# Kernel optimization log

Hardware: AMD Instinct MI355X
Metric: run time of the kernel (lower is better)

The kernel has to match this reference:

```python
import jax, jax.numpy as jnp
import numpy as np

EPS = 1e-3  # tfa LayerNormLSTMCell default norm epsilon

def _ln(z, g, b):
    # layernorm over last axis, per gate: z [B,4,U], g/b [4,U]
    mu = jnp.mean(z, axis=-1, keepdims=True)
    var = jnp.mean((z - mu) ** 2, axis=-1, keepdims=True)
    return g * (z - mu) * jax.lax.rsqrt(var + EPS) + b

def setup_inputs() -> dict:
    key = jax.random.key(0)
    ks = jax.random.split(key, 12)
    B, T, D, U, C = 1024, 100, 300, 512, 14
    sc = lambda k, shape, fan: jax.random.normal(k, shape, jnp.float32) * (1.0 / np.sqrt(fan))
    return {
        "x": jax.random.normal(ks[0], (B, T, D), jnp.float32),
        "mask": jax.random.randint(ks[1], (B, T), 0, 2).astype(jnp.int32),
        # layer 0 (input dim D)
        "W0": sc(ks[2], (D, 4 * U), D), "U0": sc(ks[3], (U, 4 * U), U),
        "b0": jnp.zeros((4 * U,), jnp.float32),
        "g0": jnp.ones((4, U), jnp.float32), "be0": jnp.zeros((4, U), jnp.float32),
        # layer 1 (input dim U)
        "W1": sc(ks[4], (U, 4 * U), U), "U1": sc(ks[5], (U, 4 * U), U),
        "b1": jnp.zeros((4 * U,), jnp.float32),
        "g1": jnp.ones((4, U), jnp.float32), "be1": jnp.zeros((4, U), jnp.float32),
        # dense softmax head
        "Wd": sc(ks[6], (U, C), U), "bd": jnp.zeros((C,), jnp.float32),
    }

def reference(x, mask, W0, U0, b0, g0, be0, W1, U1, b1, g1, be1, Wd, bd):
    B, T, D = x.shape
    U = W0.shape[1] // 4
    params = [(W0, U0, b0, g0, be0), (W1, U1, b1, g1, be1)]

    def step(carry, tins):
        hs, cs = carry
        xt, mt = tins                      # xt [B,D_in], mt [B]
        m = (mt > 0)[:, None]
        inp = xt
        new_hs, new_cs = [], []
        for l in range(2):
            W, Uw, b, g, be = params[l]
            z = (inp @ W + hs[l] @ Uw).reshape(B, 4, U)
            z = _ln(z, g, be) + b.reshape(4, U)
            i_g = jax.nn.sigmoid(z[:, 0])
            f_g = jax.nn.sigmoid(z[:, 1])
            c_g = jnp.tanh(z[:, 2])
            o_g = jax.nn.sigmoid(z[:, 3])
            c = f_g * cs[l] + i_g * c_g
            h = o_g * jnp.tanh(c)
            # keras RNN masking: carry state through masked steps
            h = jnp.where(m, h, hs[l])
            c = jnp.where(m, c, cs[l])
            new_hs.append(h); new_cs.append(c)
            inp = h
        return (tuple(new_hs), tuple(new_cs)), None

    z0 = jnp.zeros((B, U), x.dtype)
    carry0 = ((z0, z0), (z0, z0))
    xs = (jnp.swapaxes(x, 0, 1), mask.T)   # time-major [T,B,...]
    (hs, _), _ = jax.lax.scan(step, carry0, xs)
    h_top = hs[-1]                          # [B,U] = last valid output via mask carry
    return jax.nn.softmax(h_top @ Wd + bd, axis=-1)
```

## Files before the change

### kernel.cpp

```cpp
#include <hip/hip_runtime.h>


typedef _Float16 f16;
typedef _Float16 f16x8 __attribute__((ext_vector_type(8)));
typedef float f32x4 __attribute__((ext_vector_type(4)));

__global__ __launch_bounds__(256) void convert_x(
    const float* __restrict__ x, long lda, f16* __restrict__ xh, int rows) {
  int idx = blockIdx.x * 256 + threadIdx.x;
  if (idx >= rows * 320) return;
  int row = idx / 320, k = idx - row * 320;
  xh[idx] = (k < 300) ? (f16)x[(long)row * lda + k] : (f16)0.f;
}

__global__ __launch_bounds__(256) void transpose_f16(
    const float* __restrict__ W, f16* __restrict__ Bt, int K, int N, int Kp) {
  __shared__ float s[32][33];
  int n0 = blockIdx.x * 32, k0 = blockIdx.y * 32;
  int tid = threadIdx.x, c = tid & 31, r8 = tid >> 5;
  for (int rr = r8; rr < 32; rr += 8) {
    int k = k0 + rr;
    s[rr][c] = (k < K) ? W[(long)k * N + (n0 + c)] : 0.0f;
  }
  __syncthreads();
  for (int rr = r8; rr < 32; rr += 8)
    Bt[(long)(n0 + rr) * Kp + (k0 + c)] = (f16)s[c][rr];
}

__global__ __launch_bounds__(256) void gemm_f16(
    const f16* __restrict__ A1, long lda1, int K1, const f16* __restrict__ B1,
    const f16* __restrict__ A2, long lda2, int K2, const f16* __restrict__ B2,
    float* __restrict__ Zf) {
  int tid = threadIdx.x;
  int lane = tid & 63, w = tid >> 6;
  int l15 = lane & 15, quad = lane >> 4;
  long bn0 = (long)blockIdx.x * 128 + w * 32;
  long bm0 = (long)blockIdx.y * 64;

  f32x4 acc[4][2] = {};

  for (int pass = 0; pass < 2; ++pass) {
    int K = pass ? K2 : K1;
    if (K == 0) continue;
    const f16* A = pass ? A2 : A1;
    const f16* Bt = pass ? B2 : B1;
    long lda = pass ? lda2 : lda1;
    const f16* a0 = A + (bm0 + l15) * lda + quad * 8;
    const f16* b0 = Bt + (bn0 + l15) * (long)K + quad * 8;

    for (int k0 = 0; k0 < K; k0 += 32) {
      f16x8 af[4], bf[2];
#pragma unroll
      for (int i = 0; i < 4; ++i)
        af[i] = *(const f16x8*)(a0 + (long)i * 16 * lda + k0);
#pragma unroll
      for (int j = 0; j < 2; ++j)
        bf[j] = *(const f16x8*)(b0 + (long)j * 16 * K + k0);
#pragma unroll
      for (int i = 0; i < 4; ++i)
#pragma unroll
        for (int j = 0; j < 2; ++j)
          acc[i][j] = __builtin_amdgcn_mfma_f32_16x16x32_f16(af[i], bf[j], acc[i][j], 0, 0, 0);
    }
  }

#pragma unroll
  for (int i = 0; i < 4; ++i) {
    long row = bm0 + i * 16 + quad * 4;
#pragma unroll
    for (int j = 0; j < 2; ++j) {
      long col = bn0 + j * 16 + l15;
#pragma unroll
      for (int r = 0; r < 4; ++r)
        Zf[(row + r) * 2048 + col] = acc[i][j][r];
    }
  }
}

#define LOADF(AF, BF, A0, B0, K0)                          \
  AF[0] = *(const f16x8*)((A0) + (K0));                    \
  AF[1] = *(const f16x8*)((A0) + 16 * 512 + (K0));         \
  AF[2] = *(const f16x8*)((A0) + 32 * 512 + (K0));         \
  AF[3] = *(const f16x8*)((A0) + 48 * 512 + (K0));         \
  BF[0] = *(const f16x8*)((B0) + (K0));                    \
  BF[1] = *(const f16x8*)((B0) + 16 * 512 + (K0));

#define MFMAS(AF, BF)                                                                   \
  acc[0][0] = __builtin_amdgcn_mfma_f32_16x16x32_f16(AF[0], BF[0], acc[0][0], 0, 0, 0); \
  acc[0][1] = __builtin_amdgcn_mfma_f32_16x16x32_f16(AF[0], BF[1], acc[0][1], 0, 0, 0); \
  acc[1][0] = __builtin_amdgcn_mfma_f32_16x16x32_f16(AF[1], BF[0], acc[1][0], 0, 0, 0); \
  acc[1][1] = __builtin_amdgcn_mfma_f32_16x16x32_f16(AF[1], BF[1], acc[1][1], 0, 0, 0); \
  acc[2][0] = __builtin_amdgcn_mfma_f32_16x16x32_f16(AF[2], BF[0], acc[2][0], 0, 0, 0); \
  acc[2][1] = __builtin_amdgcn_mfma_f32_16x16x32_f16(AF[2], BF[1], acc[2][1], 0, 0, 0); \
  acc[3][0] = __builtin_amdgcn_mfma_f32_16x16x32_f16(AF[3], BF[0], acc[3][0], 0, 0, 0); \
  acc[3][1] = __builtin_amdgcn_mfma_f32_16x16x32_f16(AF[3], BF[1], acc[3][1], 0, 0, 0);

__global__ __launch_bounds__(256, 2) void gemm_step(
    const float* __restrict__ xt,
    const f16* __restrict__ h0, const f16* __restrict__ h1,
    const f16* __restrict__ W0t,
    const f16* __restrict__ U0t, const f16* __restrict__ W1t,
    const f16* __restrict__ U1t,
    float* __restrict__ zA, float* __restrict__ zB, int do0, int do1) {
  int prob = blockIdx.y >> 4;
  if (prob ? !do1 : !do0) return;
  int tid = threadIdx.x;
  int lane = tid & 63, w = tid >> 6;
  int l15 = lane & 15, quad = lane >> 4;
  long bn0 = (long)blockIdx.x * 128 + w * 32;
  long bm0 = (long)(blockIdx.y & 15) * 64;
  long arow = (bm0 + l15) * 512 + quad * 8;
  long brow = (bn0 + l15) * 512 + quad * 8;

  f32x4 acc[4][2] = {};

  if (prob == 0) {
    {
      const float* ax = xt + (bm0 + l15) * 30000L + quad * 8;
      const f16* bw = W0t + (bn0 + l15) * 320L + quad * 8;
#pragma unroll
      for (int k0 = 0; k0 < 288; k0 += 32) {
        f16x8 af[4], bf[2];
#pragma unroll
        for (int i = 0; i < 4; ++i) {
          f32x4 lo = *(const f32x4*)(ax + (long)i * 480000 + k0);
          f32x4 hi = *(const f32x4*)(ax + (long)i * 480000 + k0 + 4);
#pragma unroll
          for (int e = 0; e < 4; ++e) {
            af[i][e] = (f16)lo[e];
            af[i][4 + e] = (f16)hi[e];
          }
        }
        bf[0] = *(const f16x8*)(bw + k0);
        bf[1] = *(const f16x8*)(bw + 16 * 320 + k0);
        MFMAS(af, bf)
      }
      {
        f16x8 af[4], bf[2];
#pragma unroll
        for (int i = 0; i < 4; ++i) {
          long rb = (bm0 + l15 + i * 16) * 30000L;
#pragma unroll
          for (int e = 0; e < 8; ++e) {
            int k = 288 + quad * 8 + e;
            af[i][e] = (k < 300) ? (f16)xt[rb + k] : (f16)0.f;
          }
        }
        bf[0] = *(const f16x8*)(bw + 288);
        bf[1] = *(const f16x8*)(bw + 16 * 320 + 288);
        MFMAS(af, bf)
      }
    }
    {
      const f16* a0 = h0 + arow;
      const f16* b0 = U0t + brow;
      f16x8 af0[4], bf0[2], af1[4], bf1[2];
      LOADF(af0, bf0, a0, b0, 0)
      for (int k0 = 0; k0 < 448; k0 += 64) {
        LOADF(af1, bf1, a0, b0, k0 + 32)
        MFMAS(af0, bf0)
        LOADF(af0, bf0, a0, b0, k0 + 64)
        MFMAS(af1, bf1)
      }
      LOADF(af1, bf1, a0, b0, 480)
      MFMAS(af0, bf0)
      MFMAS(af1, bf1)
    }
  } else {
    const f16* ax = h0 + arow;
    const f16* bx = W1t + brow;
    const f16* ay = h1 + arow;
    const f16* by = U1t + brow;
    f16x8 axf0[4], bxf0[2], axf1[4], bxf1[2];
    f16x8 ayf0[4], byf0[2], ayf1[4], byf1[2];
    LOADF(axf0, bxf0, ax, bx, 0)
    LOADF(ayf0, byf0, ay, by, 0)
    for (int k0 = 0; k0 < 448; k0 += 64) {
      LOADF(axf1, bxf1, ax, bx, k0 + 32)
      LOADF(ayf1, byf1, ay, by, k0 + 32)
      MFMAS(axf0, bxf0)
      MFMAS(ayf0, byf0)
      LOADF(axf0, bxf0, ax, bx, k0 + 64)
      LOADF(ayf0, byf0, ay, by, k0 + 64)
      MFMAS(axf1, bxf1)
      MFMAS(ayf1, byf1)
    }
    LOADF(axf1, bxf1, ax, bx, 480)
    LOADF(ayf1, byf1, ay, by, 480)
    MFMAS(axf0, bxf0)
    MFMAS(ayf0, byf0)
    MFMAS(axf1, bxf1)
    MFMAS(ayf1, byf1)
  }

  float* Z = prob ? zB : zA;
#pragma unroll
  for (int i = 0; i < 4; ++i) {
    long row = bm0 + i * 16 + quad * 4;
#pragma unroll
    for (int j = 0; j < 2; ++j) {
      long col = bn0 + j * 16 + l15;
#pragma unroll
      for (int r = 0; r < 4; ++r)
        Z[(row + r) * 2048 + col] = acc[i][j][r];
    }
  }
}

__global__ __launch_bounds__(256) void ln_gates(
    const float* __restrict__ z, const float* __restrict__ gamma,
    const float* __restrict__ beta, const float* __restrict__ bias,
    const int* __restrict__ mask, int t,
    f16* __restrict__ h, float* __restrict__ c) {
  __shared__ float act[2048];
  int b = blockIdx.x;
  int tid = threadIdx.x;
  int w = tid >> 6, lane = tid & 63;

  const float* zb = z + (long)b * 2048 + w * 512;
  float zv[8];
  float sum = 0.0f, sq = 0.0f;
#pragma unroll
  for (int i = 0; i < 8; ++i) {
    float v = zb[lane + 64 * i];
    zv[i] = v;
    sum += v;
    sq += v * v;
  }
#pragma unroll
  for (int off = 32; off; off >>= 1) {
    sum += __shfl_xor(sum, off);
    sq += __shfl_xor(sq, off);
  }
  float mu = sum * (1.0f / 512.0f);
  float var = sq * (1.0f / 512.0f) - mu * mu;
  float is = rsqrtf(var + 1e-3f);

#pragma unroll
  for (int i = 0; i < 8; ++i) {
    int k = lane + 64 * i;
    float val = gamma[w * 512 + k] * (zv[i] - mu) * is + beta[w * 512 + k] + bias[w * 512 + k];
    float a;
    if (w == 2) {
      a = 2.0f / (1.0f + __expf(-2.0f * val)) - 1.0f;
    } else {
      a = 1.0f / (1.0f + __expf(-val));
    }
    act[w * 512 + k] = a;
  }
  __syncthreads();

  bool m = mask[(long)b * 100 + t] > 0;
#pragma unroll
  for (int i = 0; i < 2; ++i) {
    int u = tid + 256 * i;
    float co = c[(long)b * 512 + u];
    float ho = (float)h[(long)b * 512 + u];
    float cn = act[512 + u] * co + act[u] * act[1024 + u];
    float th = 2.0f / (1.0f + __expf(-2.0f * cn)) - 1.0f;
    float hn = act[1536 + u] * th;
    h[(long)b * 512 + u] = (f16)(m ? hn : ho);
    c[(long)b * 512 + u] = m ? cn : co;
  }
}

__global__ __launch_bounds__(256) void ln_gates2(
    const float* __restrict__ zA, const float* __restrict__ zB,
    const float* __restrict__ g0, const float* __restrict__ be0,
    const float* __restrict__ b0, const float* __restrict__ g1,
    const float* __restrict__ be1, const float* __restrict__ b1,
    const int* __restrict__ mask, int t,
    f16* __restrict__ h0, float* __restrict__ c0,
    f16* __restrict__ h1, float* __restrict__ c1, int do0, int do1) {
  __shared__ float act[2048];
  int layer = blockIdx.x >> 10;
  if (layer ? !do1 : !do0) return;
  int b = blockIdx.x & 1023;
  const float* z = layer ? zB : zA;
  const float* gamma = layer ? g1 : g0;
  const float* beta = layer ? be1 : be0;
  const float* bias = layer ? b1 : b0;
  f16* h = layer ? h1 : h0;
  float* c = layer ? c1 : c0;
  int tm = layer ? (t - 1) : t;

  int tid = threadIdx.x;
  int w = tid >> 6, lane = tid & 63;

  const float* zb = z + (long)b * 2048 + w * 512;
  float zv[8];
  float sum = 0.0f, sq = 0.0f;
#pragma unroll
  for (int i = 0; i < 8; ++i) {
    float v = zb[lane + 64 * i];
    zv[i] = v;
    sum += v;
    sq += v * v;
  }
#pragma unroll
  for (int off = 32; off; off >>= 1) {
    sum += __shfl_xor(sum, off);
    sq += __shfl_xor(sq, off);
  }
  float mu = sum * (1.0f / 512.0f);
  float var = sq * (1.0f / 512.0f) - mu * mu;
  float is = rsqrtf(var + 1e-3f);

#pragma unroll
  for (int i = 0; i < 8; ++i) {
    int k = lane + 64 * i;
    float val = gamma[w * 512 + k] * (zv[i] - mu) * is + beta[w * 512 + k] + bias[w * 512 + k];
    float a;
    if (w == 2) {
      a = 2.0f / (1.0f + __expf(-2.0f * val)) - 1.0f;
    } else {
      a = 1.0f / (1.0f + __expf(-val));
    }
    act[w * 512 + k] = a;
  }
  __syncthreads();

  bool m = mask[(long)b * 100 + tm] > 0;
#pragma unroll
  for (int i = 0; i < 2; ++i) {
    int u = tid + 256 * i;
    float co = c[(long)b * 512 + u];
    float ho = (float)h[(long)b * 512 + u];
    float cn = act[512 + u] * co + act[u] * act[1024 + u];
    float th = 2.0f / (1.0f + __expf(-2.0f * cn)) - 1.0f;
    float hn = act[1536 + u] * th;
    h[(long)b * 512 + u] = (f16)(m ? hn : ho);
    c[(long)b * 512 + u] = m ? cn : co;
  }
}

__global__ __launch_bounds__(64) void head_kernel(
    const f16* __restrict__ h, const float* __restrict__ Wd,
    const float* __restrict__ bd, float* __restrict__ out) {
  __shared__ float hs[512];
  __shared__ float lg[16];
  int b = blockIdx.x, tid = threadIdx.x;
#pragma unroll
  for (int i = 0; i < 8; ++i) hs[tid + 64 * i] = (float)h[(long)b * 512 + tid + 64 * i];
  __syncthreads();
  if (tid < 14) {
    float s = bd[tid];
    for (int k = 0; k < 512; ++k) s += hs[k] * Wd[k * 14 + tid];
    lg[tid] = s;
  }
  __syncthreads();
  if (tid < 14) {
    float mx = lg[0];
#pragma unroll
    for (int i = 1; i < 14; ++i) mx = fmaxf(mx, lg[i]);
    float e = __expf(lg[tid] - mx);
    float den = 0.0f;
#pragma unroll
    for (int i = 0; i < 14; ++i) den += __expf(lg[i] - mx);
    out[(long)b * 14 + tid] = e / den;
  }
}

extern "C" void kernel_launch(void* const* d_in, const int* in_sizes, int n_in,
                              void* d_out, int out_size, void* d_ws, size_t ws_size,
                              hipStream_t stream) {
  const float* x   = (const float*)d_in[0];
  const int* mask  = (const int*)d_in[1];
  const float* W0  = (const float*)d_in[2];
  const float* U0w = (const float*)d_in[3];
  const float* b0  = (const float*)d_in[4];
  const float* g0  = (const float*)d_in[5];
  const float* be0 = (const float*)d_in[6];
  const float* W1  = (const float*)d_in[7];
  const float* U1w = (const float*)d_in[8];
  const float* b1  = (const float*)d_in[9];
  const float* g1  = (const float*)d_in[10];
  const float* be1 = (const float*)d_in[11];
  const float* Wd  = (const float*)d_in[12];
  const float* bd  = (const float*)d_in[13];
  float* out = (float*)d_out;

  char* p = (char*)d_ws;
  f16*   h0  = (f16*)(p + 0);
  f16*   h1  = (f16*)(p + ((size_t)1 << 20));
  float* c0  = (float*)(p + ((size_t)2 << 20));
  float* c1  = (float*)(p + ((size_t)4 << 20));
  float* zA  = (float*)(p + ((size_t)6 << 20));
  f16*   W0t = (f16*)(p + ((size_t)14 << 20));
  f16*   U0t = (f16*)(p + ((size_t)14 << 20) + 1310720);
  f16*   W1t = (f16*)(p + ((size_t)14 << 20) + 1310720 + 2097152);
  f16*   U1t = (f16*)(p + ((size_t)14 << 20) + 1310720 + 2 * 2097152);
  float* zB  = (float*)(p + ((size_t)22 << 20));
  f16*   xh  = (f16*)(p + ((size_t)22 << 20));

  const bool pipe = ws_size >= ((size_t)30 << 20);

  hipMemsetAsync(p, 0, (size_t)6 << 20, stream);

  transpose_f16<<<dim3(64, 10), 256, 0, stream>>>(W0,  W0t, 300, 2048, 320);
  transpose_f16<<<dim3(64, 16), 256, 0, stream>>>(U0w, U0t, 512, 2048, 512);
  transpose_f16<<<dim3(64, 16), 256, 0, stream>>>(W1,  W1t, 512, 2048, 512);
  transpose_f16<<<dim3(64, 16), 256, 0, stream>>>(U1w, U1t, 512, 2048, 512);

  if (pipe) {
    for (int t = 0; t <= 100; ++t) {
      int do0 = (t < 100) ? 1 : 0;
      int do1 = (t >= 1) ? 1 : 0;
      gemm_step<<<dim3(16, 32), 256, 0, stream>>>(
          x + (long)t * 300, h0, h1, W0t, U0t, W1t, U1t, zA, zB, do0, do1);
      ln_gates2<<<2048, 256, 0, stream>>>(
          zA, zB, g0, be0, b0, g1, be1, b1, mask, t, h0, c0, h1, c1, do0, do1);
    }
  } else {
    for (int t = 0; t < 100; ++t) {
      convert_x<<<(1024 * 320 + 255) / 256, 256, 0, stream>>>(x + (long)t * 300, 30000, xh, 1024);
      gemm_f16<<<dim3(16, 16), 256, 0, stream>>>(
          xh, 320, 320, W0t, h0, 512, 512, U0t, zA);
      ln_gates<<<1024, 256, 0, stream>>>(zA, g0, be0, b0, mask, t, h0, c0);
      gemm_f16<<<dim3(16, 16), 256, 0, stream>>>(
          h0, 512, 512, W1t, h1, 512, 512, U1t, zA);
      ln_gates<<<1024, 256, 0, stream>>>(zA, g1, be1, b1, mask, t, h1, c1);
    }
  }

  head_kernel<<<1024, 64, 0, stream>>>(h1, Wd, bd, out);
}
```

Before: 5.768 ms.

## Hoist layer-0 input projection out of recurrence and fuse layer-1 weights

```diff
diff --git a/kernel.cpp b/kernel.cpp
--- a/kernel.cpp
+++ b/kernel.cpp
@@ -5,16 +5,9 @@
 typedef _Float16 f16x8 __attribute__((ext_vector_type(8)));
 typedef float f32x4 __attribute__((ext_vector_type(4)));
 
-__global__ __launch_bounds__(256) void convert_x(
-    const float* __restrict__ x, long lda, f16* __restrict__ xh, int rows) {
-  int idx = blockIdx.x * 256 + threadIdx.x;
-  if (idx >= rows * 320) return;
-  int row = idx / 320, k = idx - row * 320;
-  xh[idx] = (k < 300) ? (f16)x[(long)row * lda + k] : (f16)0.f;
-}
-
 __global__ __launch_bounds__(256) void transpose_f16(
-    const float* __restrict__ W, f16* __restrict__ Bt, int K, int N, int Kp) {
+    const float* __restrict__ W, f16* __restrict__ Bt, int K, int N, int Kp,
+    int k_off) {
   __shared__ float s[32][33];
   int n0 = blockIdx.x * 32, k0 = blockIdx.y * 32;
   int tid = threadIdx.x, c = tid & 31, r8 = tid >> 5;
@@ -24,66 +17,8 @@
   }
   __syncthreads();
   for (int rr = r8; rr < 32; rr += 8)
-    Bt[(long)(n0 + rr) * Kp + (k0 + c)] = (f16)s[c][rr];
-}
-
-__global__ __launch_bounds__(256) void gemm_f16(
-    const f16* __restrict__ A1, long lda1, int K1, const f16* __restrict__ B1,
-    const f16* __restrict__ A2, long lda2, int K2, const f16* __restrict__ B2,
-    float* __restrict__ Zf) {
-  int tid = threadIdx.x;
-  int lane = tid & 63, w = tid >> 6;
-  int l15 = lane & 15, quad = lane >> 4;
-  long bn0 = (long)blockIdx.x * 128 + w * 32;
-  long bm0 = (long)blockIdx.y * 64;
-
-  f32x4 acc[4][2] = {};
-
-  for (int pass = 0; pass < 2; ++pass) {
-    int K = pass ? K2 : K1;
-    if (K == 0) continue;
-    const f16* A = pass ? A2 : A1;
-    const f16* Bt = pass ? B2 : B1;
-    long lda = pass ? lda2 : lda1;
-    const f16* a0 = A + (bm0 + l15) * lda + quad * 8;
-    const f16* b0 = Bt + (bn0 + l15) * (long)K + quad * 8;
-
-    for (int k0 = 0; k0 < K; k0 += 32) {
-      f16x8 af[4], bf[2];
-#pragma unroll
-      for (int i = 0; i < 4; ++i)
-        af[i] = *(const f16x8*)(a0 + (long)i * 16 * lda + k0);
-#pragma unroll
-      for (int j = 0; j < 2; ++j)
-        bf[j] = *(const f16x8*)(b0 + (long)j * 16 * K + k0);
-#pragma unroll
-      for (int i = 0; i < 4; ++i)
-#pragma unroll
-        for (int j = 0; j < 2; ++j)
-          acc[i][j] = __builtin_amdgcn_mfma_f32_16x16x32_f16(af[i], bf[j], acc[i][j], 0, 0, 0);
-    }
-  }
-
-#pragma unroll
-  for (int i = 0; i < 4; ++i) {
-    long row = bm0 + i * 16 + quad * 4;
-#pragma unroll
-    for (int j = 0; j < 2; ++j) {
-      long col = bn0 + j * 16 + l15;
-#pragma unroll
-      for (int r = 0; r < 4; ++r)
-        Zf[(row + r) * 2048 + col] = acc[i][j][r];
-    }
-  }
-}
-
-#define LOADF(AF, BF, A0, B0, K0)                          \
-  AF[0] = *(const f16x8*)((A0) + (K0));                    \
-  AF[1] = *(const f16x8*)((A0) + 16 * 512 + (K0));         \
-  AF[2] = *(const f16x8*)((A0) + 32 * 512 + (K0));         \
-  AF[3] = *(const f16x8*)((A0) + 48 * 512 + (K0));         \
-  BF[0] = *(const f16x8*)((B0) + (K0));                    \
-  BF[1] = *(const f16x8*)((B0) + 16 * 512 + (K0));
+    Bt[(long)(n0 + rr) * Kp + k_off + (k0 + c)] = (f16)s[c][rr];
+}
 
 #define MFMAS(AF, BF)                                                                   \
   acc[0][0] = __builtin_amdgcn_mfma_f32_16x16x32_f16(AF[0], BF[0], acc[0][0], 0, 0, 0); \
@@ -95,12 +30,83 @@
   acc[3][0] = __builtin_amdgcn_mfma_f32_16x16x32_f16(AF[3], BF[0], acc[3][0], 0, 0, 0); \
   acc[3][1] = __builtin_amdgcn_mfma_f32_16x16x32_f16(AF[3], BF[1], acc[3][1], 0, 0, 0);
 
+#define LOADAB(AF, BF, A0, B0, LDB, K0)                    \
+  AF[0] = *(const f16x8*)((A0) + (K0));                    \
+  AF[1] = *(const f16x8*)((A0) + 16 * 1024 + (K0));        \
+  AF[2] = *(const f16x8*)((A0) + 32 * 1024 + (K0));        \
+  AF[3] = *(const f16x8*)((A0) + 48 * 1024 + (K0));        \
+  BF[0] = *(const f16x8*)((B0) + (K0));                    \
+  BF[1] = *(const f16x8*)((B0) + 16 * (LDB) + (K0));
+
+#define LOADX(AF, BF, K0)                                            \
+  {                                                                  \
+    _Pragma("unroll") for (int i = 0; i < 4; ++i) {                  \
+      f32x4 lo = *(const f32x4*)(ax + (long)i * 4800 + (K0));        \
+      f32x4 hi = *(const f32x4*)(ax + (long)i * 4800 + (K0) + 4);    \
+      _Pragma("unroll") for (int e = 0; e < 4; ++e) {                \
+        AF[i][e] = (f16)lo[e];                                       \
+        AF[i][4 + e] = (f16)hi[e];                                   \
+      }                                                              \
+    }                                                                \
+    BF[0] = *(const f16x8*)(bw + (K0));                              \
+    BF[1] = *(const f16x8*)(bw + 16 * 320 + (K0));                   \
+  }
+
+__global__ __launch_bounds__(256) void gemm_x0(
+    const float* __restrict__ x, const f16* __restrict__ W0t,
+    f16* __restrict__ z0x) {
+  int tid = threadIdx.x;
+  int lane = tid & 63, w = tid >> 6;
+  int l15 = lane & 15, quad = lane >> 4;
+  long bn0 = (long)blockIdx.x * 128 + w * 32;
+  long bm0 = (long)blockIdx.y * 64;
+  const float* ax = x + (bm0 + l15) * 300L + quad * 8;
+  const f16* bw = W0t + (bn0 + l15) * 320L + quad * 8;
+
+  f32x4 acc[4][2] = {};
+  f16x8 af0[4], bf0[2], af1[4], bf1[2];
+  LOADX(af0, bf0, 0)
+  for (int k0 = 0; k0 < 224; k0 += 64) {
+    LOADX(af1, bf1, k0 + 32)
+    MFMAS(af0, bf0)
+    LOADX(af0, bf0, k0 + 64)
+    MFMAS(af1, bf1)
+  }
+  {
+#pragma unroll
+    for (int i = 0; i < 4; ++i) {
+      long rb = (bm0 + l15 + i * 16) * 300L;
+#pragma unroll
+      for (int e = 0; e < 8; ++e) {
+        int k = 288 + quad * 8 + e;
+        af1[i][e] = (k < 300) ? (f16)x[rb + k] : (f16)0.f;
+      }
+    }
+    bf1[0] = *(const f16x8*)(bw + 288);
+    bf1[1] = *(const f16x8*)(bw + 16 * 320 + 288);
+  }
+  MFMAS(af0, bf0)
+  MFMAS(af1, bf1)
+
+#pragma unroll
+  for (int i = 0; i < 4; ++i) {
+#pragma unroll
+    for (int j = 0; j < 2; ++j) {
+      long col = bn0 + j * 16 + l15;
+#pragma unroll
+      for (int r = 0; r < 4; ++r) {
+        unsigned rr = (unsigned)(bm0 + i * 16 + quad * 4 + r);
+        unsigned b = rr / 100u, t = rr - b * 100u;
+        z0x[(long)t * 2097152 + (long)b * 2048 + col] = (f16)acc[i][j][r];
+      }
+    }
+  }
+}
+
 __global__ __launch_bounds__(256, 2) void gemm_step(
-    const float* __restrict__ xt,
-    const f16* __restrict__ h0, const f16* __restrict__ h1,
-    const f16* __restrict__ W0t,
-    const f16* __restrict__ U0t, const f16* __restrict__ W1t,
-    const f16* __restrict__ U1t,
+    const float* __restrict__ xt, const f16* __restrict__ h01,
+    const f16* __restrict__ W0t, const f16* __restrict__ U0t,
+    const f16* __restrict__ WU1t, const f16* __restrict__ cin0,
     float* __restrict__ zA, float* __restrict__ zB, int do0, int do1) {
   int prob = blockIdx.y >> 4;
   if (prob ? !do1 : !do0) return;
@@ -109,13 +115,12 @@
   int l15 = lane & 15, quad = lane >> 4;
   long bn0 = (long)blockIdx.x * 128 + w * 32;
   long bm0 = (long)(blockIdx.y & 15) * 64;
-  long arow = (bm0 + l15) * 512 + quad * 8;
-  long brow = (bn0 + l15) * 512 + quad * 8;
+  long arow = (bm0 + l15) * 1024 + quad * 8;
 
   f32x4 acc[4][2] = {};
 
   if (prob == 0) {
-    {
+    if (!cin0) {
       const float* ax = xt + (bm0 + l15) * 30000L + quad * 8;
       const f16* bw = W0t + (bn0 + l15) * 320L + quad * 8;
 #pragma unroll
@@ -152,45 +157,34 @@
       }
     }
     {
-      const f16* a0 = h0 + arow;
-      const f16* b0 = U0t + brow;
+      const f16* a0 = h01 + arow;
+      const f16* b0 = U0t + (bn0 + l15) * 512L + quad * 8;
       f16x8 af0[4], bf0[2], af1[4], bf1[2];
-      LOADF(af0, bf0, a0, b0, 0)
+      LOADAB(af0, bf0, a0, b0, 512, 0)
       for (int k0 = 0; k0 < 448; k0 += 64) {
-        LOADF(af1, bf1, a0, b0, k0 + 32)
+        LOADAB(af1, bf1, a0, b0, 512, k0 + 32)
         MFMAS(af0, bf0)
-        LOADF(af0, bf0, a0, b0, k0 + 64)
+        LOADAB(af0, bf0, a0, b0, 512, k0 + 64)
         MFMAS(af1, bf1)
       }
-      LOADF(af1, bf1, a0, b0, 480)
+      LOADAB(af1, bf1, a0, b0, 512, 480)
       MFMAS(af0, bf0)
       MFMAS(af1, bf1)
     }
   } else {
-    const f16* ax = h0 + arow;
-    const f16* bx = W1t + brow;
-    const f16* ay = h1 + arow;
-    const f16* by = U1t + brow;
-    f16x8 axf0[4], bxf0[2], axf1[4], bxf1[2];
-    f16x8 ayf0[4], byf0[2], ayf1[4], byf1[2];
-    LOADF(axf0, bxf0, ax, bx, 0)
-    LOADF(ayf0, byf0, ay, by, 0)
-    for (int k0 = 0; k0 < 448; k0 += 64) {
-      LOADF(axf1, bxf1, ax, bx, k0 + 32)
-      LOADF(ayf1, byf1, ay, by, k0 + 32)
-      MFMAS(axf0, bxf0)
-      MFMAS(ayf0, byf0)
-      LOADF(axf0, bxf0, ax, bx, k0 + 64)
-      LOADF(ayf0, byf0, ay, by, k0 + 64)
-      MFMAS(axf1, bxf1)
-      MFMAS(ayf1, byf1)
-    }
-    LOADF(axf1, bxf1, ax, bx, 480)
-    LOADF(ayf1, byf1, ay, by, 480)
-    MFMAS(axf0, bxf0)
-    MFMAS(ayf0, byf0)
-    MFMAS(axf1, bxf1)
-    MFMAS(ayf1, byf1)
+    const f16* a0 = h01 + arow;
+    const f16* b0 = WU1t + (bn0 + l15) * 1024L + quad * 8;
+    f16x8 af0[4], bf0[2], af1[4], bf1[2];
+    LOADAB(af0, bf0, a0, b0, 1024, 0)
+    for (int k0 = 0; k0 < 960; k0 += 64) {
+      LOADAB(af1, bf1, a0, b0, 1024, k0 + 32)
+      MFMAS(af0, bf0)
+      LOADAB(af0, bf0, a0, b0, 1024, k0 + 64)
+      MFMAS(af1, bf1)
+    }
+    LOADAB(af1, bf1, a0, b0, 1024, 992)
+    MFMAS(af0, bf0)
+    MFMAS(af1, bf1)
   }
 
   float* Z = prob ? zB : zA;
@@ -201,19 +195,35 @@
     for (int j = 0; j < 2; ++j) {
       long col = bn0 + j * 16 + l15;
 #pragma unroll
-      for (int r = 0; r < 4; ++r)
-        Z[(row + r) * 2048 + col] = acc[i][j][r];
-    }
-  }
-}
-
-__global__ __launch_bounds__(256) void ln_gates(
-    const float* __restrict__ z, const float* __restrict__ gamma,
-    const float* __restrict__ beta, const float* __restrict__ bias,
+      for (int r = 0; r < 4; ++r) {
+        float v = acc[i][j][r];
+        if (prob == 0 && cin0) v += (float)cin0[(row + r) * 2048 + col];
+        Z[(row + r) * 2048 + col] = v;
+      }
+    }
+  }
+}
+
+__global__ __launch_bounds__(256) void ln_gates2(
+    const float* __restrict__ zA, const float* __restrict__ zB,
+    const float* __restrict__ g0, const float* __restrict__ be0,
+    const float* __restrict__ b0, const float* __restrict__ g1,
+    const float* __restrict__ be1, const float* __restrict__ b1,
     const int* __restrict__ mask, int t,
-    f16* __restrict__ h, float* __restrict__ c) {
+    f16* __restrict__ h01, float* __restrict__ c0, float* __restrict__ c1,
+    int do0, int do1) {
   __shared__ float act[2048];
-  int b = blockIdx.x;
+  int layer = blockIdx.x >> 10;
+  if (layer ? !do1 : !do0) return;
+  int b = blockIdx.x & 1023;
+  const float* z = layer ? zB : zA;
+  const float* gamma = layer ? g1 : g0;
+  const float* beta = layer ? be1 : be0;
+  const float* bias = layer ? b1 : b0;
+  f16* h = h01 + layer * 512;
+  float* c = layer ? c1 : c0;
+  int tm = layer ? (t - 1) : t;
+
   int tid = threadIdx.x;
   int w = tid >> 6, lane = tid & 63;
 
@@ -250,98 +260,29 @@
   }
   __syncthreads();
 
-  bool m = mask[(long)b * 100 + t] > 0;
+  bool m = mask[(long)b * 100 + tm] > 0;
 #pragma unroll
   for (int i = 0; i < 2; ++i) {
     int u = tid + 256 * i;
     float co = c[(long)b * 512 + u];
-    float ho = (float)h[(long)b * 512 + u];
+    float ho = (float)h[(long)b * 1024 + u];
     float cn = act[512 + u] * co + act[u] * act[1024 + u];
     float th = 2.0f / (1.0f + __expf(-2.0f * cn)) - 1.0f;
     float hn = act[1536 + u] * th;
-    h[(long)b * 512 + u] = (f16)(m ? hn : ho);
+    h[(long)b * 1024 + u] = (f16)(m ? hn : ho);
     c[(long)b * 512 + u] = m ? cn : co;
   }
 }
 
-__global__ __launch_bounds__(256) void ln_gates2(
-    const float* __restrict__ zA, const float* __restrict__ zB,
-    const float* __restrict__ g0, const float* __restrict__ be0,
-    const float* __restrict__ b0, const float* __restrict__ g1,
-    const float* __restrict__ be1, const float* __restrict__ b1,
-    const int* __restrict__ mask, int t,
-    f16* __restrict__ h0, float* __restrict__ c0,
-    f16* __restrict__ h1, float* __restrict__ c1, int do0, int do1) {
-  __shared__ float act[2048];
-  int layer = blockIdx.x >> 10;
-  if (layer ? !do1 : !do0) return;
-  int b = blockIdx.x & 1023;
-  const float* z = layer ? zB : zA;
-  const float* gamma = layer ? g1 : g0;
-  const float* beta = layer ? be1 : be0;
-  const float* bias = layer ? b1 : b0;
-  f16* h = layer ? h1 : h0;
-  float* c = layer ? c1 : c0;
-  int tm = layer ? (t - 1) : t;
-
-  int tid = threadIdx.x;
-  int w = tid >> 6, lane = tid & 63;
-
-  const float* zb = z + (long)b * 2048 + w * 512;
-  float zv[8];
-  float sum = 0.0f, sq = 0.0f;
-#pragma unroll
-  for (int i = 0; i < 8; ++i) {
-    float v = zb[lane + 64 * i];
-    zv[i] = v;
-    sum += v;
-    sq += v * v;
-  }
-#pragma unroll
-  for (int off = 32; off; off >>= 1) {
-    sum += __shfl_xor(sum, off);
-    sq += __shfl_xor(sq, off);
-  }
-  float mu = sum * (1.0f / 512.0f);
-  float var = sq * (1.0f / 512.0f) - mu * mu;
-  float is = rsqrtf(var + 1e-3f);
-
-#pragma unroll
-  for (int i = 0; i < 8; ++i) {
-    int k = lane + 64 * i;
-    float val = gamma[w * 512 + k] * (zv[i] - mu) * is + beta[w * 512 + k] + bias[w * 512 + k];
-    float a;
-    if (w == 2) {
-      a = 2.0f / (1.0f + __expf(-2.0f * val)) - 1.0f;
-    } else {
-      a = 1.0f / (1.0f + __expf(-val));
-    }
-    act[w * 512 + k] = a;
-  }
-  __syncthreads();
-
-  bool m = mask[(long)b * 100 + tm] > 0;
-#pragma unroll
-  for (int i = 0; i < 2; ++i) {
-    int u = tid + 256 * i;
-    float co = c[(long)b * 512 + u];
-    float ho = (float)h[(long)b * 512 + u];
-    float cn = act[512 + u] * co + act[u] * act[1024 + u];
-    float th = 2.0f / (1.0f + __expf(-2.0f * cn)) - 1.0f;
-    float hn = act[1536 + u] * th;
-    h[(long)b * 512 + u] = (f16)(m ? hn : ho);
-    c[(long)b * 512 + u] = m ? cn : co;
-  }
-}
-
 __global__ __launch_bounds__(64) void head_kernel(
-    const f16* __restrict__ h, const float* __restrict__ Wd,
+    const f16* __restrict__ h01, const float* __restrict__ Wd,
     const float* __restrict__ bd, float* __restrict__ out) {
   __shared__ float hs[512];
   __shared__ float lg[16];
   int b = blockIdx.x, tid = threadIdx.x;
 #pragma unroll
-  for (int i = 0; i < 8; ++i) hs[tid + 64 * i] = (float)h[(long)b * 512 + tid + 64 * i];
+  for (int i = 0; i < 8; ++i)
+    hs[tid + 64 * i] = (float)h01[(long)b * 1024 + 512 + tid + 64 * i];
   __syncthreads();
   if (tid < 14) {
     float s = bd[tid];
@@ -381,47 +322,39 @@
   float* out = (float*)d_out;
 
   char* p = (char*)d_ws;
-  f16*   h0  = (f16*)(p + 0);
-  f16*   h1  = (f16*)(p + ((size_t)1 << 20));
-  float* c0  = (float*)(p + ((size_t)2 << 20));
-  float* c1  = (float*)(p + ((size_t)4 << 20));
-  float* zA  = (float*)(p + ((size_t)6 << 20));
-  f16*   W0t = (f16*)(p + ((size_t)14 << 20));
-  f16*   U0t = (f16*)(p + ((size_t)14 << 20) + 1310720);
-  f16*   W1t = (f16*)(p + ((size_t)14 << 20) + 1310720 + 2097152);
-  f16*   U1t = (f16*)(p + ((size_t)14 << 20) + 1310720 + 2 * 2097152);
-  float* zB  = (float*)(p + ((size_t)22 << 20));
-  f16*   xh  = (f16*)(p + ((size_t)22 << 20));
-
-  const bool pipe = ws_size >= ((size_t)30 << 20);
-
-  hipMemsetAsync(p, 0, (size_t)6 << 20, stream);
-
-  transpose_f16<<<dim3(64, 10), 256, 0, stream>>>(W0,  W0t, 300, 2048, 320);
-  transpose_f16<<<dim3(64, 16), 256, 0, stream>>>(U0w, U0t, 512, 2048, 512);
-  transpose_f16<<<dim3(64, 16), 256, 0, stream>>>(W1,  W1t, 512, 2048, 512);
-  transpose_f16<<<dim3(64, 16), 256, 0, stream>>>(U1w, U1t, 512, 2048, 512);
-
-  if (pipe) {
-    for (int t = 0; t <= 100; ++t) {
-      int do0 = (t < 100) ? 1 : 0;
-      int do1 = (t >= 1) ? 1 : 0;
-      gemm_step<<<dim3(16, 32), 256, 0, stream>>>(
-          x + (long)t * 300, h0, h1, W0t, U0t, W1t, U1t, zA, zB, do0, do1);
-      ln_gates2<<<2048, 256, 0, stream>>>(
-          zA, zB, g0, be0, b0, g1, be1, b1, mask, t, h0, c0, h1, c1, do0, do1);
-    }
-  } else {
-    for (int t = 0; t < 100; ++t) {
-      convert_x<<<(1024 * 320 + 255) / 256, 256, 0, stream>>>(x + (long)t * 300, 30000, xh, 1024);
-      gemm_f16<<<dim3(16, 16), 256, 0, stream>>>(
-          xh, 320, 320, W0t, h0, 512, 512, U0t, zA);
-      ln_gates<<<1024, 256, 0, stream>>>(zA, g0, be0, b0, mask, t, h0, c0);
-      gemm_f16<<<dim3(16, 16), 256, 0, stream>>>(
-          h0, 512, 512, W1t, h1, 512, 512, U1t, zA);
-      ln_gates<<<1024, 256, 0, stream>>>(zA, g1, be1, b1, mask, t, h1, c1);
-    }
-  }
-
-  head_kernel<<<1024, 64, 0, stream>>>(h1, Wd, bd, out);
-}
+  const size_t MB = (size_t)1 << 20;
+  f16*   h01  = (f16*)(p + 0);
+  float* c0   = (float*)(p + 2 * MB);
+  float* c1   = (float*)(p + 4 * MB);
+  float* zA   = (float*)(p + 6 * MB);
+  float* zB   = (float*)(p + 14 * MB);
+  f16*   W0t  = (f16*)(p + 22 * MB);
+  f16*   U0t  = (f16*)(p + 22 * MB + 1310720);
+  f16*   WU1t = (f16*)(p + 22 * MB + 1310720 + 2097152);
+  f16*   z0x  = (f16*)(p + 32 * MB);
+
+  const bool hoist = ws_size >= (size_t)432 * MB;
+
+  hipMemsetAsync(p, 0, 6 * MB, stream);
+
+  transpose_f16<<<dim3(64, 10), 256, 0, stream>>>(W0,  W0t, 300, 2048, 320, 0);
+  transpose_f16<<<dim3(64, 16), 256, 0, stream>>>(U0w, U0t, 512, 2048, 512, 0);
+  transpose_f16<<<dim3(64, 16), 256, 0, stream>>>(W1,  WU1t, 512, 2048, 1024, 0);
+  transpose_f16<<<dim3(64, 16), 256, 0, stream>>>(U1w, WU1t, 512, 2048, 1024, 512);
+
+  if (hoist) {
+    gemm_x0<<<dim3(16, 1600), 256, 0, stream>>>(x, W0t, z0x);
+  }
+
+  for (int t = 0; t <= 100; ++t) {
+    int do0 = (t < 100) ? 1 : 0;
+    int do1 = (t >= 1) ? 1 : 0;
+    const f16* cin0 = hoist ? (z0x + (long)t * 2097152) : nullptr;
+    gemm_step<<<dim3(16, 32), 256, 0, stream>>>(
+        x + (long)t * 300, h01, W0t, U0t, WU1t, cin0, zA, zB, do0, do1);
+    ln_gates2<<<2048, 256, 0, stream>>>(
+        zA, zB, g0, be0, b0, g1, be1, b1, mask, t, h01, c0, c1, do0, do1);
+  }
+
+  head_kernel<<<1024, 64, 0, stream>>>(h01, Wd, bd, out);
+}
```

Result: slower. 6.468 ms (+12.1%).
